# Optimization experiments

Measured on AMD Instinct MI355X. Metric: run time of the kernel, lower is better.

The kernel has to match this reference:

```python
import jax, jax.numpy as jnp
import numpy as np

INPUT_SIZE = 1024
HIDDEN_SIZE = 1024
W_RANK = 64
U_RANK = 64
BATCH = 32768


def setup_inputs() -> dict:
    key = jax.random.key(0)
    ks = jax.random.split(key, 16)
    p = lambda k, shape: 0.1 * jax.random.normal(k, shape, dtype=jnp.float32)
    return {
        "x": jax.random.normal(ks[0], (BATCH, INPUT_SIZE), dtype=jnp.float32),
        "h": jax.random.normal(ks[1], (BATCH, HIDDEN_SIZE), dtype=jnp.float32),
        "W": p(ks[2], (INPUT_SIZE, W_RANK)),
        "W1": p(ks[3], (W_RANK, HIDDEN_SIZE)),
        "W2": p(ks[4], (W_RANK, HIDDEN_SIZE)),
        "W3": p(ks[5], (W_RANK, HIDDEN_SIZE)),
        "U": p(ks[6], (HIDDEN_SIZE, U_RANK)),
        "U1": p(ks[7], (U_RANK, HIDDEN_SIZE)),
        "U2": p(ks[8], (U_RANK, HIDDEN_SIZE)),
        "U3": p(ks[9], (U_RANK, HIDDEN_SIZE)),
        "U1_diag": p(ks[10], (HIDDEN_SIZE,)),
        "U2_diag": p(ks[11], (HIDDEN_SIZE,)),
        "U3_diag": p(ks[12], (HIDDEN_SIZE,)),
        "bias_r": jnp.ones((1, HIDDEN_SIZE), dtype=jnp.float32),
        "bias_gate": jnp.ones((1, HIDDEN_SIZE), dtype=jnp.float32),
        "bias_update": jnp.ones((1, HIDDEN_SIZE), dtype=jnp.float32),
    }


def reference(x, h, W, W1, W2, W3, U, U1, U2, U3,
              U1_diag, U2_diag, U3_diag, bias_r, bias_gate, bias_update):
    # Low-rank projections shared across gates (matches torch matmul order)
    xW = x @ W          # [B, wRank]
    hU = h @ U          # [B, uRank]
    wVal1 = xW @ W1
    wVal2 = xW @ W2
    wVal3 = xW @ W3
    uVal1 = hU @ U1
    uVal2 = hU @ U2
    r = jax.nn.sigmoid(wVal1 + uVal1 + h * U1_diag + bias_r)
    z = jax.nn.sigmoid(wVal2 + uVal2 + h * U2_diag + bias_gate)
    rh = r * h
    matVal_c = wVal3 + (rh @ U) @ U3 + rh * U3_diag
    c_tilda = jnp.tanh(matVal_c + bias_update)
    h_next = z * h + (1.0 - z) * c_tilda
    return h_next
```

## Files before the change

kernel.cpp:

```cpp
#include <hip/hip_runtime.h>
#include <hip/hip_bf16.h>


typedef __attribute__((ext_vector_type(8))) short short8;
typedef __attribute__((ext_vector_type(4))) float f32x4;
typedef __attribute__((ext_vector_type(4))) float f4;

#define WS_UT   65536
#define WS_P1T  131072
#define WS_P2T  262144
#define WS_P3T  393216
#define WS_A12  524288
#define WS_RHU  4718592

__device__ __forceinline__ short f2bf(float f) {
  unsigned u = __builtin_bit_cast(unsigned, f);
  u += 0x7FFFu + ((u >> 16) & 1u);
  return (short)(u >> 16);
}
__device__ __forceinline__ short8 cvt8(f4 a, f4 b) {
  short8 r;
#pragma unroll
  for (int j = 0; j < 4; ++j) { r[j] = f2bf(a[j]); r[4 + j] = f2bf(b[j]); }
  return r;
}
__device__ __forceinline__ f32x4 mfma16(short8 a, short8 b, f32x4 c) {
  return __builtin_amdgcn_mfma_f32_16x16x32_bf16(a, b, c, 0, 0, 0);
}
__device__ __forceinline__ short8 ldg8(const short* p) {
  return *reinterpret_cast<const short8*>(p);
}
__device__ __forceinline__ f4 ldf4(const float* p) {
  return *reinterpret_cast<const f4*>(p);
}

__device__ __forceinline__ void cp16(void* l, const void* g) {
  __builtin_amdgcn_global_load_lds(
      (const __attribute__((address_space(1))) void*)g,
      (__attribute__((address_space(3))) void*)l, 16, 0, 0);
}
#define VWAIT(N) do { asm volatile("s_waitcnt vmcnt(" #N ")" ::: "memory"); \
                      __builtin_amdgcn_sched_barrier(0); } while (0)

__device__ __forceinline__ short8 rd128s(const short* b, int row, int col) {
  return *reinterpret_cast<const short8*>(b + row * 128 + (col ^ ((row & 7) << 3)));
}
__device__ __forceinline__ void wr128s(short* b, int row, int col8, short8 v) {
  *reinterpret_cast<short8*>(b + row * 128 + (col8 ^ ((row & 7) << 3))) = v;
}
__device__ __forceinline__ void wr64(short* b, int row, int col, short v) {
  b[row * 64 + (col ^ ((row & 7) << 3))] = v;
}
__device__ __forceinline__ short8 rd64(const short* b, int row, int col) {
  return *reinterpret_cast<const short8*>(b + row * 64 + (col ^ ((row & 7) << 3)));
}

#define LOG2E 1.4426950408889634f
__device__ __forceinline__ float sigm_f(float v) {
  return __builtin_amdgcn_rcpf(1.f + __builtin_amdgcn_exp2f(-v * LOG2E));
}
__device__ __forceinline__ float tanh_f(float v) {
  float t = __builtin_amdgcn_exp2f(v * (2.f * LOG2E));
  return 1.f - 2.f * __builtin_amdgcn_rcpf(t + 1.f);
}

__global__ void prep_kernel(const float* __restrict__ W,  const float* __restrict__ W1,
                            const float* __restrict__ W2, const float* __restrict__ W3,
                            const float* __restrict__ U,  const float* __restrict__ U1,
                            const float* __restrict__ U2, const float* __restrict__ U3,
                            short* __restrict__ ws) {
  int i = blockIdx.x * blockDim.x + threadIdx.x;
  float v;
  if (i < 65536) {
    int n = i >> 10, k = i & 1023;
    v = W[k * 64 + n];
  } else if (i < 131072) {
    int j = i - 65536;
    int n = j >> 10, k = j & 1023;
    v = U[k * 64 + n];
  } else {
    int j = i - 131072;
    int sel = j >> 17;
    int jj = j & 131071;
    int n = jj >> 7, k = jj & 127;
    const float* Wk = sel == 0 ? W1 : sel == 1 ? W2 : W3;
    const float* Uk = sel == 0 ? U1 : sel == 1 ? U2 : U3;
    v = (k < 64) ? Wk[k * 1024 + n] : Uk[(k - 64) * 1024 + n];
  }
  ws[i] = f2bf(v);
}

__global__ __launch_bounds__(512, 1) void k1_a12(
    const float* __restrict__ x, const float* __restrict__ h,
    const short* __restrict__ ws, short* __restrict__ A12) {
  __shared__ __align__(16) short sW[64 * 1024];

  const int tid = threadIdx.x;
  const int w = tid >> 6, l = tid & 63, l15 = l & 15, lg = l >> 4;
  const int m  = blockIdx.x & 1;
  const int rc = blockIdx.x >> 1;
  const int sr = rc * 128 + w * 16;
  const float* src = m ? h : x;
  const short* Bt  = ws + m * WS_UT;

#pragma unroll
  for (int rnd = 0; rnd < 16; ++rnd) {
    const int byte = rnd * 8192 + tid * 16;
    const int row  = byte >> 11;
    const int col  = byte & 2047;
    const int scol = col ^ ((row & 7) << 4);
    cp16((char*)sW + byte, (const char*)(Bt + row * 1024) + scol);
  }
  VWAIT(0);
  __syncthreads();

  auto rdW = [&](int row, int kcol) {
    const int byte = row * 2048 + ((kcol * 2) ^ ((row & 7) << 4));
    return *reinterpret_cast<const short8*>((const char*)sW + byte);
  };

  const float* xr = src + (size_t)(sr + l15) * 1024 + lg * 8;

  f4 ring[8][2];
#pragma unroll
  for (int i = 0; i < 8; ++i) {
    ring[i][0] = ldf4(xr + i * 32);
    ring[i][1] = ldf4(xr + i * 32 + 4);
  }

  f32x4 acc[4] = {};
#pragma unroll
  for (int c = 0; c < 32; ++c) {
    if (c < 25)      VWAIT(14);
    else if (c == 25) VWAIT(12);
    else if (c == 26) VWAIT(10);
    else if (c == 27) VWAIT(8);
    else if (c == 28) VWAIT(6);
    else if (c == 29) VWAIT(4);
    else if (c == 30) VWAIT(2);
    else              VWAIT(0);

    short8 av = cvt8(ring[c & 7][0], ring[c & 7][1]);
    const int kcol = c * 32 + lg * 8;
#pragma unroll
    for (int cf = 0; cf < 4; ++cf)
      acc[cf] = mfma16(av, rdW(cf * 16 + l15, kcol), acc[cf]);

    if (c < 24) {
      ring[c & 7][0] = ldf4(xr + (c + 8) * 32);
      ring[c & 7][1] = ldf4(xr + (c + 8) * 32 + 4);
    }
  }

#pragma unroll
  for (int cf = 0; cf < 4; ++cf)
#pragma unroll
    for (int j = 0; j < 4; ++j)
      A12[(size_t)(sr + lg * 4 + j) * 128 + m * 64 + cf * 16 + l15] = f2bf(acc[cf][j]);
}

__global__ __launch_bounds__(256, 4) void k23_rhu(
    const float* __restrict__ h, const float* __restrict__ u1d,
    const float* __restrict__ biasR,
    const short* __restrict__ ws, const short* __restrict__ A12,
    short* __restrict__ rhU) {
  const short* Ut  = ws + WS_UT;
  const short* P1t = ws + WS_P1T;
  __shared__ __align__(16) short sT[4][2][16 * 64];
  __shared__ __align__(16) float sRed[2][2][16 * 64];

  const int tid = threadIdx.x;
  const int w   = tid >> 6, l = tid & 63, l15 = l & 15, lg = l >> 4;
  const int s   = w >> 1;
  const int ch  = w & 1;
  const int sr  = blockIdx.x * 32 + s * 16;

  short8 a12[4];
#pragma unroll
  for (int k0 = 0; k0 < 4; ++k0)
    a12[k0] = ldg8(A12 + (size_t)(sr + l15) * 128 + k0 * 32 + lg * 8);

  f32x4 accU[4] = {};
#pragma unroll 1
  for (int tt = 0; tt < 8; ++tt) {
    const int n0 = ch * 512 + tt * 64;

    float hv[4][4];
#pragma unroll
    for (int cf = 0; cf < 4; ++cf)
#pragma unroll
      for (int j = 0; j < 4; ++j)
        hv[cf][j] = h[(size_t)(sr + lg * 4 + j) * 1024 + n0 + cf * 16 + l15];

    f32x4 accR[4] = {};
#pragma unroll
    for (int k0 = 0; k0 < 4; ++k0)
#pragma unroll
      for (int cf = 0; cf < 4; ++cf)
        accR[cf] = mfma16(a12[k0],
            ldg8(P1t + (size_t)(n0 + cf * 16 + l15) * 128 + k0 * 32 + lg * 8),
            accR[cf]);

    short* sw = &sT[w][tt & 1][0];
#pragma unroll
    for (int cf = 0; cf < 4; ++cf) {
      const int cc = n0 + cf * 16 + l15;
      const float d1 = u1d[cc], b_r = biasR[cc];
#pragma unroll
      for (int j = 0; j < 4; ++j) {
        float rv = sigm_f(accR[cf][j] + hv[cf][j] * d1 + b_r);
        wr64(sw, lg * 4 + j, cf * 16 + l15, f2bf(rv * hv[cf][j]));
      }
    }
    short8 arh0 = rd64(sw, l15, lg * 8);
    short8 arh1 = rd64(sw, l15, 32 + lg * 8);
#pragma unroll
    for (int cf = 0; cf < 4; ++cf)
      accU[cf] = mfma16(arh0,
          ldg8(Ut + (size_t)(cf * 16 + l15) * 1024 + n0 + lg * 8), accU[cf]);
#pragma unroll
    for (int cf = 0; cf < 4; ++cf)
      accU[cf] = mfma16(arh1,
          ldg8(Ut + (size_t)(cf * 16 + l15) * 1024 + n0 + 32 + lg * 8), accU[cf]);
  }

  {
    float* fT = &sRed[s][ch][0];
#pragma unroll
    for (int cf = 0; cf < 4; ++cf)
#pragma unroll
      for (int j = 0; j < 4; ++j) {
        int row = lg * 4 + j, col = cf * 16 + l15;
        fT[row * 64 + (col ^ ((row & 7) << 2))] = accU[cf][j];
      }
  }
  __syncthreads();
  if (ch == 0) {
    const float* f0 = &sRed[s][0][0];
    const float* f1 = &sRed[s][1][0];
#pragma unroll
    for (int cf = 0; cf < 4; ++cf)
#pragma unroll
      for (int j = 0; j < 4; ++j) {
        int row = lg * 4 + j, col = cf * 16 + l15;
        int idx = row * 64 + (col ^ ((row & 7) << 2));
        rhU[(size_t)(sr + row) * 64 + col] = f2bf(f0[idx] + f1[idx]);
      }
  }
}

__global__ __launch_bounds__(256, 2) void k4_out(
    const float* __restrict__ h,
    const float* __restrict__ u1d, const float* __restrict__ u2d,
    const float* __restrict__ u3d,
    const float* __restrict__ biasR, const float* __restrict__ biasZ,
    const float* __restrict__ biasU,
    const short* __restrict__ ws, const short* __restrict__ A12,
    const short* __restrict__ rhU, float* __restrict__ out) {
  __shared__ __align__(16) short sB1[64 * 128], sB2[64 * 128], sB3[64 * 128];
  __shared__ __align__(16) float hS[2][4][16 * 64];

  const int tid = threadIdx.x;
  const int w = tid >> 6, l = tid & 63, l15 = l & 15, lg = l >> 4;
  const int ct = blockIdx.x & 15, rc = blockIdx.x >> 4;
  const int n0 = ct * 64;

#pragma unroll
  for (int mat = 0; mat < 3; ++mat) {
    const short* srcw = (mat == 0) ? (ws + WS_P1T) : (mat == 1) ? (ws + WS_P2T) : (ws + WS_P3T);
    short* dst = (mat == 0) ? sB1 : (mat == 1) ? sB2 : sB3;
#pragma unroll
    for (int i = 0; i < 4; ++i) {
      int id = tid + i * 256;
      int row = id >> 4, gc = id & 15;
      wr128s(dst, row, gc * 8, ldg8(srcw + (size_t)(n0 + row) * 128 + gc * 8));
    }
  }
  float d1_[4], d2_[4], d3_[4], br_[4], bz_[4], bu_[4];
#pragma unroll
  for (int cf = 0; cf < 4; ++cf) {
    const int cc = n0 + cf * 16 + l15;
    d1_[cf] = u1d[cc]; d2_[cf] = u2d[cc]; d3_[cf] = u3d[cc];
    br_[cf] = biasR[cc]; bz_[cf] = biasZ[cc]; bu_[cf] = biasU[cc];
  }
  __syncthreads();

  const int srow = l >> 4;
  const int slin = (l & 15) * 16;
  auto STAGE = [&](int rnd, int b) {
    const int sb = rc * 512 + rnd * 64 + w * 16;
#pragma unroll
    for (int i = 0; i < 4; ++i) {
      int r = i * 4 + srow;
      int kb = slin ^ ((r & 7) << 4);
      cp16((char*)&hS[b][w][0] + i * 1024,
           (const char*)(h + (size_t)(sb + r) * 1024 + n0) + kb);
    }
  };

  STAGE(0, 0);
#pragma unroll 1
  for (int rnd = 0; rnd < 8; ++rnd) {
    const int sr = rc * 512 + rnd * 64 + w * 16;
    short8 a12[4], arhu[2];
#pragma unroll
    for (int k0 = 0; k0 < 4; ++k0)
      a12[k0] = ldg8(A12 + (size_t)(sr + l15) * 128 + k0 * 32 + lg * 8);
#pragma unroll
    for (int kk = 0; kk < 2; ++kk)
      arhu[kk] = ldg8(rhU + (size_t)(sr + l15) * 64 + kk * 32 + lg * 8);
    if (rnd < 7) { STAGE(rnd + 1, (rnd + 1) & 1); VWAIT(4); }
    else         { VWAIT(0); }
    const char* H = (const char*)&hS[rnd & 1][w][0];

    float hv[4][4];
#pragma unroll
    for (int cf = 0; cf < 4; ++cf)
#pragma unroll
      for (int j = 0; j < 4; ++j) {
        int rr = lg * 4 + j;
        hv[cf][j] = *(const float*)(H + rr * 256 + ((cf * 64 + l15 * 4) ^ ((rr & 7) << 4)));
      }

    f32x4 aR[4] = {}, aZ[4] = {}, aC[4] = {};
#pragma unroll
    for (int k0 = 0; k0 < 4; ++k0) {
      const short8 a3 = (k0 < 2) ? a12[k0] : arhu[k0 - 2];
#pragma unroll
      for (int cf = 0; cf < 4; ++cf) {
        aR[cf] = mfma16(a12[k0], rd128s(sB1, cf * 16 + l15, k0 * 32 + lg * 8), aR[cf]);
        aZ[cf] = mfma16(a12[k0], rd128s(sB2, cf * 16 + l15, k0 * 32 + lg * 8), aZ[cf]);
        aC[cf] = mfma16(a3,      rd128s(sB3, cf * 16 + l15, k0 * 32 + lg * 8), aC[cf]);
      }
    }
#pragma unroll
    for (int cf = 0; cf < 4; ++cf) {
      const int cc = n0 + cf * 16 + l15;
#pragma unroll
      for (int j = 0; j < 4; ++j) {
        const size_t gi = (size_t)(sr + lg * 4 + j) * 1024 + cc;
        const float hvj = hv[cf][j];
        float rv = sigm_f(aR[cf][j] + hvj * d1_[cf] + br_[cf]);
        float zv = sigm_f(aZ[cf][j] + hvj * d2_[cf] + bz_[cf]);
        float cv = tanh_f(aC[cf][j] + rv * hvj * d3_[cf] + bu_[cf]);
        out[gi] = zv * hvj + (1.f - zv) * cv;
      }
    }
  }
}

extern "C" void kernel_launch(void* const* d_in, const int* in_sizes, int n_in,
                              void* d_out, int out_size, void* d_ws, size_t ws_size,
                              hipStream_t stream) {
  const float* x   = (const float*)d_in[0];
  const float* h   = (const float*)d_in[1];
  const float* W   = (const float*)d_in[2];
  const float* W1  = (const float*)d_in[3];
  const float* W2  = (const float*)d_in[4];
  const float* W3  = (const float*)d_in[5];
  const float* U   = (const float*)d_in[6];
  const float* U1  = (const float*)d_in[7];
  const float* U2  = (const float*)d_in[8];
  const float* U3  = (const float*)d_in[9];
  const float* u1d = (const float*)d_in[10];
  const float* u2d = (const float*)d_in[11];
  const float* u3d = (const float*)d_in[12];
  const float* bR  = (const float*)d_in[13];
  const float* bZ  = (const float*)d_in[14];
  const float* bU  = (const float*)d_in[15];
  short* ws  = (short*)d_ws;
  short* A12 = ws + WS_A12;
  short* rhU = ws + WS_RHU;

  prep_kernel<<<2048, 256, 0, stream>>>(W, W1, W2, W3, U, U1, U2, U3, ws);
  k1_a12<<<512, 512, 0, stream>>>(x, h, ws, A12);
  k23_rhu<<<1024, 256, 0, stream>>>(h, u1d, bR, ws, A12, rhU);
  k4_out<<<1024, 256, 0, stream>>>(h, u1d, u2d, u3d, bR, bZ, bU, ws, A12, rhU, (float*)d_out);
}
```

Measured before the change: 214.9 us.

## Fuse rh·U reduction and output gate kernels into one row-block kernel

Merges the rhU kernel and the output kernel into a single kernel in which each block owns 32 rows: it computes the rh@U reduction, combines the halves in shared memory to form the rhU operand in registers, then loops over the columns to produce the output. This removes the rhU workspace round-trip and one launch. In exchange, the output phase reads the P1/P2/P3 weights directly from global/L2 instead of staging them in LDS, and h is re-read from global without async LDS staging. The R gate matmul is also recomputed in both phases.

```diff
diff --git a/kernel.cpp b/kernel.cpp
--- a/kernel.cpp
+++ b/kernel.cpp
@@ -11,7 +11,6 @@
 #define WS_P2T  262144
 #define WS_P3T  393216
 #define WS_A12  524288
-#define WS_RHU  4718592
 
 __device__ __forceinline__ short f2bf(float f) {
   unsigned u = __builtin_bit_cast(unsigned, f);
@@ -42,12 +41,6 @@
 #define VWAIT(N) do { asm volatile("s_waitcnt vmcnt(" #N ")" ::: "memory"); \
                       __builtin_amdgcn_sched_barrier(0); } while (0)
 
-__device__ __forceinline__ short8 rd128s(const short* b, int row, int col) {
-  return *reinterpret_cast<const short8*>(b + row * 128 + (col ^ ((row & 7) << 3)));
-}
-__device__ __forceinline__ void wr128s(short* b, int row, int col8, short8 v) {
-  *reinterpret_cast<short8*>(b + row * 128 + (col8 ^ ((row & 7) << 3))) = v;
-}
 __device__ __forceinline__ void wr64(short* b, int row, int col, short v) {
   b[row * 64 + (col ^ ((row & 7) << 3))] = v;
 }
@@ -159,168 +152,118 @@
       A12[(size_t)(sr + lg * 4 + j) * 128 + m * 64 + cf * 16 + l15] = f2bf(acc[cf][j]);
 }
 
-__global__ __launch_bounds__(256, 4) void k23_rhu(
-    const float* __restrict__ h, const float* __restrict__ u1d,
-    const float* __restrict__ biasR,
-    const short* __restrict__ ws, const short* __restrict__ A12,
-    short* __restrict__ rhU) {
-  const short* Ut  = ws + WS_UT;
-  const short* P1t = ws + WS_P1T;
-  __shared__ __align__(16) short sT[4][2][16 * 64];
-  __shared__ __align__(16) float sRed[2][2][16 * 64];
-
-  const int tid = threadIdx.x;
-  const int w   = tid >> 6, l = tid & 63, l15 = l & 15, lg = l >> 4;
-  const int s   = w >> 1;
-  const int ch  = w & 1;
-  const int sr  = blockIdx.x * 32 + s * 16;
-
-  short8 a12[4];
-#pragma unroll
-  for (int k0 = 0; k0 < 4; ++k0)
-    a12[k0] = ldg8(A12 + (size_t)(sr + l15) * 128 + k0 * 32 + lg * 8);
-
-  f32x4 accU[4] = {};
-#pragma unroll 1
-  for (int tt = 0; tt < 8; ++tt) {
-    const int n0 = ch * 512 + tt * 64;
-
-    float hv[4][4];
-#pragma unroll
-    for (int cf = 0; cf < 4; ++cf)
-#pragma unroll
-      for (int j = 0; j < 4; ++j)
-        hv[cf][j] = h[(size_t)(sr + lg * 4 + j) * 1024 + n0 + cf * 16 + l15];
-
-    f32x4 accR[4] = {};
-#pragma unroll
-    for (int k0 = 0; k0 < 4; ++k0)
-#pragma unroll
-      for (int cf = 0; cf < 4; ++cf)
-        accR[cf] = mfma16(a12[k0],
-            ldg8(P1t + (size_t)(n0 + cf * 16 + l15) * 128 + k0 * 32 + lg * 8),
-            accR[cf]);
-
-    short* sw = &sT[w][tt & 1][0];
-#pragma unroll
-    for (int cf = 0; cf < 4; ++cf) {
-      const int cc = n0 + cf * 16 + l15;
-      const float d1 = u1d[cc], b_r = biasR[cc];
-#pragma unroll
-      for (int j = 0; j < 4; ++j) {
-        float rv = sigm_f(accR[cf][j] + hv[cf][j] * d1 + b_r);
-        wr64(sw, lg * 4 + j, cf * 16 + l15, f2bf(rv * hv[cf][j]));
-      }
-    }
-    short8 arh0 = rd64(sw, l15, lg * 8);
-    short8 arh1 = rd64(sw, l15, 32 + lg * 8);
-#pragma unroll
-    for (int cf = 0; cf < 4; ++cf)
-      accU[cf] = mfma16(arh0,
-          ldg8(Ut + (size_t)(cf * 16 + l15) * 1024 + n0 + lg * 8), accU[cf]);
-#pragma unroll
-    for (int cf = 0; cf < 4; ++cf)
-      accU[cf] = mfma16(arh1,
-          ldg8(Ut + (size_t)(cf * 16 + l15) * 1024 + n0 + 32 + lg * 8), accU[cf]);
-  }
-
-  {
-    float* fT = &sRed[s][ch][0];
-#pragma unroll
-    for (int cf = 0; cf < 4; ++cf)
-#pragma unroll
-      for (int j = 0; j < 4; ++j) {
-        int row = lg * 4 + j, col = cf * 16 + l15;
-        fT[row * 64 + (col ^ ((row & 7) << 2))] = accU[cf][j];
-      }
-  }
-  __syncthreads();
-  if (ch == 0) {
-    const float* f0 = &sRed[s][0][0];
-    const float* f1 = &sRed[s][1][0];
-#pragma unroll
-    for (int cf = 0; cf < 4; ++cf)
-#pragma unroll
-      for (int j = 0; j < 4; ++j) {
-        int row = lg * 4 + j, col = cf * 16 + l15;
-        int idx = row * 64 + (col ^ ((row & 7) << 2));
-        rhU[(size_t)(sr + row) * 64 + col] = f2bf(f0[idx] + f1[idx]);
-      }
-  }
-}
-
-__global__ __launch_bounds__(256, 2) void k4_out(
+__global__ __launch_bounds__(256, 3) void k234(
     const float* __restrict__ h,
     const float* __restrict__ u1d, const float* __restrict__ u2d,
     const float* __restrict__ u3d,
     const float* __restrict__ biasR, const float* __restrict__ biasZ,
     const float* __restrict__ biasU,
     const short* __restrict__ ws, const short* __restrict__ A12,
-    const short* __restrict__ rhU, float* __restrict__ out) {
-  __shared__ __align__(16) short sB1[64 * 128], sB2[64 * 128], sB3[64 * 128];
-  __shared__ __align__(16) float hS[2][4][16 * 64];
+    float* __restrict__ out) {
+  const short* Ut  = ws + WS_UT;
+  const short* P1t = ws + WS_P1T;
+  const short* P2t = ws + WS_P2T;
+  const short* P3t = ws + WS_P3T;
+  __shared__ __align__(16) short sT[4][2][16 * 64];
+  __shared__ __align__(16) float sRed[2][2][16 * 64];
 
   const int tid = threadIdx.x;
-  const int w = tid >> 6, l = tid & 63, l15 = l & 15, lg = l >> 4;
-  const int ct = blockIdx.x & 15, rc = blockIdx.x >> 4;
-  const int n0 = ct * 64;
-
-#pragma unroll
-  for (int mat = 0; mat < 3; ++mat) {
-    const short* srcw = (mat == 0) ? (ws + WS_P1T) : (mat == 1) ? (ws + WS_P2T) : (ws + WS_P3T);
-    short* dst = (mat == 0) ? sB1 : (mat == 1) ? sB2 : sB3;
-#pragma unroll
-    for (int i = 0; i < 4; ++i) {
-      int id = tid + i * 256;
-      int row = id >> 4, gc = id & 15;
-      wr128s(dst, row, gc * 8, ldg8(srcw + (size_t)(n0 + row) * 128 + gc * 8));
-    }
-  }
-  float d1_[4], d2_[4], d3_[4], br_[4], bz_[4], bu_[4];
-#pragma unroll
-  for (int cf = 0; cf < 4; ++cf) {
-    const int cc = n0 + cf * 16 + l15;
-    d1_[cf] = u1d[cc]; d2_[cf] = u2d[cc]; d3_[cf] = u3d[cc];
-    br_[cf] = biasR[cc]; bz_[cf] = biasZ[cc]; bu_[cf] = biasU[cc];
+  const int w   = tid >> 6, l = tid & 63, l15 = l & 15, lg = l >> 4;
+  const int s   = w >> 1;
+  const int ch  = w & 1;
+  const int sr  = blockIdx.x * 32 + s * 16;
+
+  short8 a12[4];
+#pragma unroll
+  for (int k0 = 0; k0 < 4; ++k0)
+    a12[k0] = ldg8(A12 + (size_t)(sr + l15) * 128 + k0 * 32 + lg * 8);
+
+  f32x4 accU[4] = {};
+#pragma unroll 1
+  for (int tt = 0; tt < 8; ++tt) {
+    const int n0 = ch * 512 + tt * 64;
+
+    float hv[4][4];
+#pragma unroll
+    for (int cf = 0; cf < 4; ++cf)
+#pragma unroll
+      for (int j = 0; j < 4; ++j)
+        hv[cf][j] = h[(size_t)(sr + lg * 4 + j) * 1024 + n0 + cf * 16 + l15];
+
+    f32x4 accR[4] = {};
+#pragma unroll
+    for (int k0 = 0; k0 < 4; ++k0)
+#pragma unroll
+      for (int cf = 0; cf < 4; ++cf)
+        accR[cf] = mfma16(a12[k0],
+            ldg8(P1t + (size_t)(n0 + cf * 16 + l15) * 128 + k0 * 32 + lg * 8),
+            accR[cf]);
+
+    short* sw = &sT[w][tt & 1][0];
+#pragma unroll
+    for (int cf = 0; cf < 4; ++cf) {
+      const int cc = n0 + cf * 16 + l15;
+      const float d1 = u1d[cc], b_r = biasR[cc];
+#pragma unroll
+      for (int j = 0; j < 4; ++j) {
+        float rv = sigm_f(accR[cf][j] + hv[cf][j] * d1 + b_r);
+        wr64(sw, lg * 4 + j, cf * 16 + l15, f2bf(rv * hv[cf][j]));
+      }
+    }
+    short8 arh0 = rd64(sw, l15, lg * 8);
+    short8 arh1 = rd64(sw, l15, 32 + lg * 8);
+#pragma unroll
+    for (int cf = 0; cf < 4; ++cf)
+      accU[cf] = mfma16(arh0,
+          ldg8(Ut + (size_t)(cf * 16 + l15) * 1024 + n0 + lg * 8), accU[cf]);
+#pragma unroll
+    for (int cf = 0; cf < 4; ++cf)
+      accU[cf] = mfma16(arh1,
+          ldg8(Ut + (size_t)(cf * 16 + l15) * 1024 + n0 + 32 + lg * 8), accU[cf]);
+  }
+
+  {
+    float* fT = &sRed[s][ch][0];
+#pragma unroll
+    for (int cf = 0; cf < 4; ++cf)
+#pragma unroll
+      for (int j = 0; j < 4; ++j) {
+        int row = lg * 4 + j, col = cf * 16 + l15;
+        fT[row * 64 + (col ^ ((row & 7) << 2))] = accU[cf][j];
+      }
   }
   __syncthreads();
 
-  const int srow = l >> 4;
-  const int slin = (l & 15) * 16;
-  auto STAGE = [&](int rnd, int b) {
-    const int sb = rc * 512 + rnd * 64 + w * 16;
-#pragma unroll
-    for (int i = 0; i < 4; ++i) {
-      int r = i * 4 + srow;
-      int kb = slin ^ ((r & 7) << 4);
-      cp16((char*)&hS[b][w][0] + i * 1024,
-           (const char*)(h + (size_t)(sb + r) * 1024 + n0) + kb);
-    }
-  };
-
-  STAGE(0, 0);
+  short8 arhu[2];
+  {
+    const float* f0 = &sRed[s][0][0];
+    const float* f1 = &sRed[s][1][0];
+    const int sw2 = (l15 & 7) << 2;
+#pragma unroll
+    for (int kk = 0; kk < 2; ++kk) {
+      const int c0 = kk * 32 + lg * 8;
+      f4 pa = *reinterpret_cast<const f4*>(f0 + l15 * 64 + (c0 ^ sw2));
+      f4 pb = *reinterpret_cast<const f4*>(f0 + l15 * 64 + ((c0 + 4) ^ sw2));
+      f4 qa = *reinterpret_cast<const f4*>(f1 + l15 * 64 + (c0 ^ sw2));
+      f4 qb = *reinterpret_cast<const f4*>(f1 + l15 * 64 + ((c0 + 4) ^ sw2));
+      arhu[kk] = cvt8(pa + qa, pb + qb);
+    }
+  }
+
 #pragma unroll 1
-  for (int rnd = 0; rnd < 8; ++rnd) {
-    const int sr = rc * 512 + rnd * 64 + w * 16;
-    short8 a12[4], arhu[2];
-#pragma unroll
-    for (int k0 = 0; k0 < 4; ++k0)
-      a12[k0] = ldg8(A12 + (size_t)(sr + l15) * 128 + k0 * 32 + lg * 8);
-#pragma unroll
-    for (int kk = 0; kk < 2; ++kk)
-      arhu[kk] = ldg8(rhU + (size_t)(sr + l15) * 64 + kk * 32 + lg * 8);
-    if (rnd < 7) { STAGE(rnd + 1, (rnd + 1) & 1); VWAIT(4); }
-    else         { VWAIT(0); }
-    const char* H = (const char*)&hS[rnd & 1][w][0];
-
-    float hv[4][4];
-#pragma unroll
-    for (int cf = 0; cf < 4; ++cf)
-#pragma unroll
-      for (int j = 0; j < 4; ++j) {
-        int rr = lg * 4 + j;
-        hv[cf][j] = *(const float*)(H + rr * 256 + ((cf * 64 + l15 * 4) ^ ((rr & 7) << 4)));
-      }
+  for (int tt = 0; tt < 8; ++tt) {
+    const int n0 = ch * 512 + tt * 64;
+
+    float hv[4][4], d1_[4], d2_[4], d3_[4], br_[4], bz_[4], bu_[4];
+#pragma unroll
+    for (int cf = 0; cf < 4; ++cf) {
+      const int cc = n0 + cf * 16 + l15;
+#pragma unroll
+      for (int j = 0; j < 4; ++j)
+        hv[cf][j] = h[(size_t)(sr + lg * 4 + j) * 1024 + cc];
+      d1_[cf] = u1d[cc]; d2_[cf] = u2d[cc]; d3_[cf] = u3d[cc];
+      br_[cf] = biasR[cc]; bz_[cf] = biasZ[cc]; bu_[cf] = biasU[cc];
+    }
 
     f32x4 aR[4] = {}, aZ[4] = {}, aC[4] = {};
 #pragma unroll
@@ -328,11 +271,13 @@
       const short8 a3 = (k0 < 2) ? a12[k0] : arhu[k0 - 2];
 #pragma unroll
       for (int cf = 0; cf < 4; ++cf) {
-        aR[cf] = mfma16(a12[k0], rd128s(sB1, cf * 16 + l15, k0 * 32 + lg * 8), aR[cf]);
-        aZ[cf] = mfma16(a12[k0], rd128s(sB2, cf * 16 + l15, k0 * 32 + lg * 8), aZ[cf]);
-        aC[cf] = mfma16(a3,      rd128s(sB3, cf * 16 + l15, k0 * 32 + lg * 8), aC[cf]);
+        const size_t bo = (size_t)(n0 + cf * 16 + l15) * 128 + k0 * 32 + lg * 8;
+        aR[cf] = mfma16(a12[k0], ldg8(P1t + bo), aR[cf]);
+        aZ[cf] = mfma16(a12[k0], ldg8(P2t + bo), aZ[cf]);
+        aC[cf] = mfma16(a3,      ldg8(P3t + bo), aC[cf]);
       }
     }
+
 #pragma unroll
     for (int cf = 0; cf < 4; ++cf) {
       const int cc = n0 + cf * 16 + l15;
@@ -370,10 +315,8 @@
   const float* bU  = (const float*)d_in[15];
   short* ws  = (short*)d_ws;
   short* A12 = ws + WS_A12;
-  short* rhU = ws + WS_RHU;
 
   prep_kernel<<<2048, 256, 0, stream>>>(W, W1, W2, W3, U, U1, U2, U3, ws);
   k1_a12<<<512, 512, 0, stream>>>(x, h, ws, A12);
-  k23_rhu<<<1024, 256, 0, stream>>>(h, u1d, bR, ws, A12, rhU);
-  k4_out<<<1024, 256, 0, stream>>>(h, u1d, u2d, u3d, bR, bZ, bU, ws, A12, rhU, (float*)d_out);
-}
+  k234<<<1024, 256, 0, stream>>>(h, u1d, u2d, u3d, bR, bZ, bU, ws, A12, (float*)d_out);
+}
```

Result: slower. 374.3 us (+74.2%).
